# Kernel tuning notes

Measured on AMD Instinct MI355X. Metric: run time of the kernel, lower is better.

The kernel has to match this reference:

```python
import jax, jax.numpy as jnp
import numpy as np
import math

B, S, H = 8, 2048, 256

def setup_inputs() -> dict:
    key = jax.random.key(0)
    ks = jax.random.split(key, 7)
    stdv = 1.0 / math.sqrt(H)
    return {
        "k": jax.random.normal(ks[0], (B, S, H), dtype=jnp.float32),
        "q": jax.random.normal(ks[1], (B, S, H), dtype=jnp.float32),
        "v": jax.random.normal(ks[2], (B, S, H), dtype=jnp.float32),
        "mask": jax.random.bernoulli(ks[3], 0.5, (B, S, S)),  # bool, masked-out positions
        "W_query": jax.random.uniform(ks[4], (H, H), jnp.float32, -stdv, stdv),
        "W_key": jax.random.uniform(ks[5], (H, H), jnp.float32, -stdv, stdv),
        "W_val": jax.random.uniform(ks[6], (H, H), jnp.float32, -stdv, stdv),
    }

def reference(k, q, v, mask, W_query, W_key, W_val):
    Q = jnp.einsum("bsh,hd->bsd", q, W_query)
    K = jnp.einsum("bsh,hd->bsd", k, W_key)
    V = jnp.einsum("bsh,hd->bsd", v, W_val)
    norm = 1.0 / math.sqrt(Q.shape[-1])
    compat = norm * jnp.einsum("bqd,bkd->bqk", Q, K)  # [B,Sq,Sk]
    compat = jnp.where(mask, -jnp.inf, compat)
    score = jax.nn.softmax(compat, axis=-1)
    score = jnp.nan_to_num(score, nan=0.0)  # fully-masked rows -> all zeros
    return jnp.einsum("bqk,bkd->bqd", score, V)
```

## Files before the change

kernel.cpp:

```cpp
#include <hip/hip_runtime.h>


#define B_ 8
#define S_ 2048
#define H_ 256

typedef __attribute__((ext_vector_type(8))) short s16x8;
typedef __attribute__((ext_vector_type(4))) float f32x4;
typedef __attribute__((ext_vector_type(4))) unsigned short u16x4;
typedef __attribute__((ext_vector_type(8))) unsigned short u16x8;

#if __has_builtin(__builtin_amdgcn_exp2f)
#define EXP2F(x) __builtin_amdgcn_exp2f(x)
#else
#define EXP2F(x) exp2f(x)
#endif
#define L2E 1.4426950408889634f

__device__ __forceinline__ unsigned short f2bf(float f) {
  unsigned int u = __builtin_bit_cast(unsigned int, f);
  u += 0x7fffu + ((u >> 16) & 1u);
  return (unsigned short)(u >> 16);
}
__device__ __forceinline__ float bf2f(unsigned short h) {
  unsigned int u = ((unsigned int)h) << 16;
  return __builtin_bit_cast(float, u);
}
__device__ __forceinline__ f32x4 mfma_bf16(s16x8 a, s16x8 b, f32x4 c) {
  return __builtin_amdgcn_mfma_f32_16x16x32_bf16(a, b, c, 0, 0, 0);
}
__device__ __forceinline__ float sel4(const float v[4], int r) {
  float t0 = (r & 1) ? v[1] : v[0];
  float t1 = (r & 1) ? v[3] : v[2];
  return (r & 2) ? t1 : t0;
}
__device__ __forceinline__ void async16(const unsigned short* g, unsigned short* l) {
  __builtin_amdgcn_global_load_lds(
      (const __attribute__((address_space(1))) unsigned int*)g,
      (__attribute__((address_space(3))) unsigned int*)l, 16, 0, 0);
}

__global__ __launch_bounds__(256) void wt_kernel(
    const float* __restrict__ Wq, const float* __restrict__ Wk,
    const float* __restrict__ Wv, unsigned short* __restrict__ Wt) {
  __shared__ unsigned short tile[64 * 72];
  int z = blockIdx.x >> 4, x = blockIdx.x & 15;
  const float* W = (z == 0) ? Wq : (z == 1) ? Wk : Wv;
  int n0 = (x & 3) * 64, h0 = (x >> 2) * 64;
  int t = threadIdx.x;
#pragma unroll
  for (int j = 0; j < 4; ++j) {
    int c = j * 256 + t;
    int i = c >> 4, ch = c & 15;
    float4 f = *(const float4*)&W[(h0 + i) * 256 + n0 + ch * 4];
    u16x4 p;
    p[0] = f2bf(f.x); p[1] = f2bf(f.y); p[2] = f2bf(f.z); p[3] = f2bf(f.w);
    *(u16x4*)&tile[i * 72 + ch * 4] = p;
  }
  __syncthreads();
#pragma unroll
  for (int j = 0; j < 2; ++j) {
    int c = j * 256 + t;
    int nr = c >> 3, ch = c & 7;
    u16x8 o;
#pragma unroll
    for (int k = 0; k < 8; ++k) o[k] = tile[(ch * 8 + k) * 72 + nr];
    *(u16x8*)&Wt[z * 65536 + (n0 + nr) * 256 + h0 + ch * 8] = o;
  }
}

__global__ __launch_bounds__(256) void fused_kernel(
    const int* __restrict__ mask, unsigned short* __restrict__ Mb,
    const float* __restrict__ Xq, const float* __restrict__ Xk,
    const float* __restrict__ Xv, const unsigned short* __restrict__ Wt,
    unsigned short* __restrict__ Qb, unsigned short* __restrict__ Kb,
    unsigned short* __restrict__ Vt) {
  __shared__ unsigned short plds[16384];

  if (blockIdx.x >= 768) {
    unsigned int g = (blockIdx.x - 768) * 256 + threadIdx.x;
    const int4* src = (const int4*)mask + (size_t)g * 4;
    unsigned int v = 0;
#pragma unroll
    for (int j = 0; j < 4; ++j) {
      int4 x = src[j];
      v |= (x.x != 0 ? 1u : 0u) << (j * 4 + 0);
      v |= (x.y != 0 ? 1u : 0u) << (j * 4 + 1);
      v |= (x.z != 0 ? 1u : 0u) << (j * 4 + 2);
      v |= (x.w != 0 ? 1u : 0u) << (j * 4 + 3);
    }
    Mb[g] = (unsigned short)v;
    return;
  }

  int z = blockIdx.x >> 8;
  int bx = blockIdx.x & 255;
  const float* X = (z == 0) ? Xq : (z == 1) ? Xk : Xv;
  const unsigned short* Wz = Wt + z * 65536;

  int t = threadIdx.x;
  int w = t >> 6, lane = t & 63, quad = lane >> 4, l15 = lane & 15;
  int m0 = bx * 64;
  const float* xrow = X + (size_t)(m0 + w * 16 + l15) * H_;

  f32x4 zero4 = {0.f, 0.f, 0.f, 0.f};
  f32x4 acc[16];
#pragma unroll
  for (int i = 0; i < 16; ++i) acc[i] = zero4;

#pragma unroll
  for (int j = 0; j < 4; ++j) {
    int c = j * 256 + t;
    int n = c >> 2, p = c & 3;
    async16(Wz + n * 256 + ((p ^ ((n >> 1) & 3)) << 3),
            plds + j * 2048 + w * 512);
  }
  float4 a0 = *(const float4*)(xrow + quad * 8);
  float4 a1 = *(const float4*)(xrow + quad * 8 + 4);

  for (int c8 = 0; c8 < 8; ++c8) {
    int cur = c8 & 1;
    unsigned short* Wc = plds + cur * 8192;
    __syncthreads();

    if (c8 < 7) {
      unsigned short* Wn = plds + (cur ^ 1) * 8192;
#pragma unroll
      for (int j = 0; j < 4; ++j) {
        int c = j * 256 + t;
        int n = c >> 2, p = c & 3;
        async16(Wz + n * 256 + (c8 + 1) * 32 + ((p ^ ((n >> 1) & 3)) << 3),
                Wn + j * 2048 + w * 512);
      }
    }
    float4 na0, na1;
    if (c8 < 7) {
      na0 = *(const float4*)(xrow + (c8 + 1) * 32 + quad * 8);
      na1 = *(const float4*)(xrow + (c8 + 1) * 32 + quad * 8 + 4);
    }
    s16x8 af;
    af[0] = (short)f2bf(a0.x); af[1] = (short)f2bf(a0.y);
    af[2] = (short)f2bf(a0.z); af[3] = (short)f2bf(a0.w);
    af[4] = (short)f2bf(a1.x); af[5] = (short)f2bf(a1.y);
    af[6] = (short)f2bf(a1.z); af[7] = (short)f2bf(a1.w);

#pragma unroll
    for (int nf = 0; nf < 16; ++nf) {
      int n = nf * 16 + l15;
      s16x8 bf = *(const s16x8*)&Wc[n * 32 + ((quad ^ ((n >> 1) & 3)) << 3)];
      acc[nf] = mfma_bf16(af, bf, acc[nf]);
    }
    a0 = na0; a1 = na1;
  }
  __syncthreads();

  float scale = (z == 0) ? 0.0625f : 1.0f;
  int b = m0 >> 11, s0 = m0 & 2047;
#pragma unroll
  for (int h = 0; h < 2; ++h) {
    if (h) __syncthreads();
    if (z < 2) {
#pragma unroll
      for (int nf2 = 0; nf2 < 8; ++nf2) {
        int n = nf2 * 16 + l15;
#pragma unroll
        for (int r = 0; r < 4; ++r)
          plds[(w * 16 + quad * 4 + r) * 136 + n] = f2bf(acc[h * 8 + nf2][r] * scale);
      }
      __syncthreads();
      unsigned short* Y = (z == 0) ? Qb : Kb;
#pragma unroll
      for (int j = 0; j < 4; ++j) {
        int c = j * 256 + t;
        int mr = c >> 4, ch = c & 15;
        u16x8 o = *(const u16x8*)&plds[mr * 136 + ch * 8];
        *(u16x8*)&Y[(size_t)(m0 + mr) * H_ + h * 128 + ch * 8] = o;
      }
    } else {
#pragma unroll
      for (int nf2 = 0; nf2 < 8; ++nf2) {
        int dl = nf2 * 16 + l15;
#pragma unroll
        for (int r = 0; r < 4; ++r)
          plds[dl * 72 + (w * 16 + quad * 4 + r)] = f2bf(acc[h * 8 + nf2][r]);
      }
      __syncthreads();
#pragma unroll
      for (int j = 0; j < 4; ++j) {
        int c = j * 256 + t;
        int dr = c >> 3, ch = c & 7;
        u16x8 o = *(const u16x8*)&plds[dr * 72 + ch * 8];
        *(u16x8*)&Vt[((size_t)b * H_ + h * 128 + dr) * S_ + s0 + ch * 8] = o;
      }
    }
  }
}

__global__ __launch_bounds__(256, 2) void attn_kernel(
    const unsigned short* __restrict__ Qb, const unsigned short* __restrict__ Kb,
    const unsigned short* __restrict__ Vt, const unsigned int* __restrict__ Mb,
    unsigned short* __restrict__ Op, float* __restrict__ Ml,
    float* __restrict__ out) {
  __shared__ unsigned short lds[35328];
  unsigned short* Ps = lds + 32768;

  int t = threadIdx.x;
  int w = t >> 6, lane = t & 63, quad = lane >> 4, l15 = lane & 15;
  int b = blockIdx.x;
  int q0 = blockIdx.y * 64;
  int split = blockIdx.z, nsplit = gridDim.z;
  int kbeg = (64 * split) / nsplit, kend = (64 * (split + 1)) / nsplit;

  s16x8 qa[8];
  {
    const unsigned short* qp =
        Qb + ((size_t)b * S_ + q0 + w * 16 + l15) * H_ + quad * 8;
#pragma unroll
    for (int c = 0; c < 8; ++c) qa[c] = *(const s16x8*)(qp + 32 * c);
  }

  const unsigned short* Kbb = Kb + (size_t)b * S_ * H_;
  const unsigned short* Vbb = Vt + (size_t)b * H_ * S_;

  int krow = lane >> 5, kch = lane & 31;
  int vrow = lane >> 2, vch = lane & 3;

  f32x4 zero4 = {0.f, 0.f, 0.f, 0.f};
  f32x4 acc[16];
#pragma unroll
  for (int i = 0; i < 16; ++i) acc[i] = zero4;
  float l_r[4] = {0.f, 0.f, 0.f, 0.f};

  const unsigned int* mrow[4];
#pragma unroll
  for (int r = 0; r < 4; ++r)
    mrow[r] = Mb + ((size_t)b * S_ + q0 + w * 16 + quad * 4 + r) * 64;

  {
    int k0 = kbeg * 32;
    unsigned short* Kd = lds;
    unsigned short* Vd = lds + 8192;
#pragma unroll
    for (int j = 0; j < 4; ++j) {
      int key = (w * 4 + j) * 2 + krow;
      async16(Kbb + ((size_t)(k0 + key) << 8) + ((kch ^ (key & 7)) << 3),
              Kd + (w * 4 + j) * 512);
      int d = w * 64 + j * 16 + vrow;
      async16(Vbb + ((size_t)d << 11) + k0 + ((vch ^ (d & 3)) << 3),
              Vd + (w * 64 + j * 16) * 32);
    }
  }
  unsigned int mw[4];
#pragma unroll
  for (int r = 0; r < 4; ++r) mw[r] = mrow[r][kbeg];

  for (int kt = kbeg; kt < kend; ++kt) {
    int cur = (kt - kbeg) & 1;
    unsigned short* Ksc = lds + cur * 16384;
    unsigned short* Vsc = Ksc + 8192;
    __syncthreads();

    if (kt + 1 < kend) {
      int k0 = (kt + 1) * 32;
      unsigned short* Kd = lds + (cur ^ 1) * 16384;
      unsigned short* Vd = Kd + 8192;
#pragma unroll
      for (int j = 0; j < 4; ++j) {
        int key = (w * 4 + j) * 2 + krow;
        async16(Kbb + ((size_t)(k0 + key) << 8) + ((kch ^ (key & 7)) << 3),
                Kd + (w * 4 + j) * 512);
        int d = w * 64 + j * 16 + vrow;
        async16(Vbb + ((size_t)d << 11) + k0 + ((vch ^ (d & 3)) << 3),
                Vd + (w * 64 + j * 16) * 32);
      }
    }
    unsigned int mwn[4];
    {
      int ktn = (kt + 1 < kend) ? kt + 1 : kt;
#pragma unroll
      for (int r = 0; r < 4; ++r) mwn[r] = mrow[r][ktn];
    }

    f32x4 sacc[2];
#pragma unroll
    for (int nf = 0; nf < 2; ++nf) sacc[nf] = zero4;
#pragma unroll
    for (int c = 0; c < 8; ++c) {
#pragma unroll
      for (int nf = 0; nf < 2; ++nf) {
        int n = nf * 16 + l15;
        s16x8 kb = *(const s16x8*)&Ksc[n * 256 + (((quad + 4 * c) ^ (n & 7)) << 3)];
        sacc[nf] = mfma_bf16(qa[c], kb, sacc[nf]);
      }
    }

    float pvv[2][4];
#pragma unroll
    for (int r = 0; r < 4; ++r) {
      unsigned int bits = mw[r] >> l15;
#pragma unroll
      for (int nf = 0; nf < 2; ++nf) {
        float p = ((bits >> (nf * 16)) & 1u)
                      ? 0.f
                      : EXP2F(sacc[nf][r] * L2E);
        pvv[nf][r] = p;
        l_r[r] += p;
      }
    }

#pragma unroll
    for (int nf = 0; nf < 2; ++nf)
#pragma unroll
      for (int r = 0; r < 4; ++r) {
        int key = nf * 16 + l15;
        int ql = quad * 4 + r;
        Ps[w * 640 + ql * 40 + key] = f2bf(pvv[nf][r]);
      }

    {
      s16x8 bp = *(const s16x8*)&Ps[w * 640 + l15 * 40 + quad * 8];
#pragma unroll
      for (int mf = 0; mf < 16; ++mf) {
        int d = mf * 16 + l15;
        s16x8 av = *(const s16x8*)&Vsc[d * 32 + ((quad ^ (d & 3)) << 3)];
        acc[mf] = mfma_bf16(av, bp, acc[mf]);
      }
    }

#pragma unroll
    for (int r = 0; r < 4; ++r) mw[r] = mwn[r];
  }

#pragma unroll
  for (int r = 0; r < 4; ++r) {
#pragma unroll
    for (int d = 1; d < 16; d <<= 1) l_r[r] += __shfl_xor(l_r[r], d, 64);
  }

  if (gridDim.z == 1) {
    float l4[4];
    int srcl = (l15 >> 2) << 4;
#pragma unroll
    for (int r = 0; r < 4; ++r) l4[r] = __shfl(l_r[r], srcl, 64);
    float lq = sel4(l4, l15 & 3);
    float linv = (lq > 0.f) ? (1.0f / lq) : 0.f;
    float* op = out + ((size_t)b * S_ + q0 + w * 16 + l15) * H_ + quad * 4;
#pragma unroll
    for (int mf = 0; mf < 16; ++mf) {
      float4 o;
      o.x = acc[mf][0] * linv; o.y = acc[mf][1] * linv;
      o.z = acc[mf][2] * linv; o.w = acc[mf][3] * linv;
      *(float4*)(op + mf * 16) = o;
    }
  } else {
    int qg = q0 + w * 16 + l15;
    unsigned short* op =
        Op + (((size_t)split * B_ + b) * S_ + qg) * H_ + quad * 4;
#pragma unroll
    for (int mf = 0; mf < 16; ++mf) {
      u16x4 pk;
      pk[0] = f2bf(acc[mf][0]); pk[1] = f2bf(acc[mf][1]);
      pk[2] = f2bf(acc[mf][2]); pk[3] = f2bf(acc[mf][3]);
      *(u16x4*)(op + mf * 16) = pk;
    }
    if (l15 == 0) {
#pragma unroll
      for (int r = 0; r < 4; ++r) {
        int qr = q0 + w * 16 + quad * 4 + r;
        Ml[((size_t)split * B_ + b) * S_ + qr] = l_r[r];
      }
    }
  }
}

__global__ __launch_bounds__(1024) void combine_kernel(
    const unsigned short* __restrict__ Op, const float* __restrict__ Ml,
    float* __restrict__ out, int nsplit) {
  int q = blockIdx.x * 4 + (threadIdx.x >> 8);
  int b = blockIdx.y, d = threadIdx.x & 255;
  float osum = 0.f, lsum = 0.f;
  for (int i = 0; i < nsplit; ++i) {
    size_t ro = ((size_t)i * B_ + b) * S_ + q;
    lsum += Ml[ro];
    osum += bf2f(Op[ro * H_ + d]);
  }
  float linv = (lsum > 0.f) ? (1.0f / lsum) : 0.f;
  out[((size_t)b * S_ + q) * H_ + d] = osum * linv;
}

extern "C" void kernel_launch(void* const* d_in, const int* in_sizes, int n_in,
                              void* d_out, int out_size, void* d_ws, size_t ws_size,
                              hipStream_t stream) {
  const float* k_in = (const float*)d_in[0];
  const float* q_in = (const float*)d_in[1];
  const float* v_in = (const float*)d_in[2];
  const int* mask = (const int*)d_in[3];
  const float* Wq = (const float*)d_in[4];
  const float* Wk = (const float*)d_in[5];
  const float* Wv = (const float*)d_in[6];
  float* out = (float*)d_out;

  unsigned short* Qb = (unsigned short*)d_ws;
  unsigned short* Kb = Qb + (size_t)4194304;
  unsigned short* Vt = Kb + (size_t)4194304;
  unsigned short* Wt = Vt + (size_t)4194304;
  unsigned short* Mb = Wt + (size_t)196608;
  unsigned short* Op = Mb + (size_t)2097152;
  float* Ml = (float*)(Op + (size_t)8388608);
  const size_t need = 46792704;
  int nsplit = (ws_size >= need) ? 2 : 1;

  hipLaunchKernelGGL(wt_kernel, dim3(48), dim3(256), 0, stream,
                     Wq, Wk, Wv, Wt);
  hipLaunchKernelGGL(fused_kernel, dim3(8960), dim3(256), 0, stream,
                     mask, Mb, q_in, k_in, v_in, Wt, Qb, Kb, Vt);
  hipLaunchKernelGGL(attn_kernel, dim3(8, 32, nsplit), dim3(256), 0, stream,
                     Qb, Kb, Vt, (const unsigned int*)Mb, Op, Ml, out);
  if (nsplit > 1)
    hipLaunchKernelGGL(combine_kernel, dim3(512, 8), dim3(1024), 0, stream,
                       Op, Ml, out, nsplit);
}
```

Before: 311.7 us.

## Single-buffer attention LDS for higher occupancy, raise split-K to 4, ballot mask packing

The attention kernel drops K/V double buffering and uses a single LDS buffer with a sync before and after each async load. This roughly halves shared memory per block, and launch bounds now ask for 4 blocks per CU. The key dimension is split into 4 parts instead of 2, which adds more partial outputs and a larger workspace for the combine kernel. The mask packing now uses coalesced per-thread loads with a wavefront ballot instead of each thread reading 16 ints. The trade-off is that load latency is no longer overlapped inside a block, relying instead on more resident blocks and a larger grid.

```diff
diff --git a/kernel.cpp b/kernel.cpp
--- a/kernel.cpp
+++ b/kernel.cpp
@@ -77,19 +77,20 @@
     unsigned short* __restrict__ Vt) {
   __shared__ unsigned short plds[16384];
 
+  int t = threadIdx.x;
+  int w = t >> 6, lane = t & 63, quad = lane >> 4, l15 = lane & 15;
+
   if (blockIdx.x >= 768) {
-    unsigned int g = (blockIdx.x - 768) * 256 + threadIdx.x;
-    const int4* src = (const int4*)mask + (size_t)g * 4;
-    unsigned int v = 0;
-#pragma unroll
-    for (int j = 0; j < 4; ++j) {
-      int4 x = src[j];
-      v |= (x.x != 0 ? 1u : 0u) << (j * 4 + 0);
-      v |= (x.y != 0 ? 1u : 0u) << (j * 4 + 1);
-      v |= (x.z != 0 ? 1u : 0u) << (j * 4 + 2);
-      v |= (x.w != 0 ? 1u : 0u) << (j * 4 + 3);
-    }
-    Mb[g] = (unsigned short)v;
+    size_t base = (size_t)(blockIdx.x - 768) * 4096;
+#pragma unroll
+    for (int s = 0; s < 16; ++s) {
+      int x = mask[base + s * 256 + t];
+      unsigned long long bm = __ballot(x != 0);
+      if (lane < 4) {
+        Mb[(base >> 4) + s * 16 + w * 4 + lane] =
+            (unsigned short)(bm >> (16 * lane));
+      }
+    }
     return;
   }
 
@@ -98,8 +99,6 @@
   const float* X = (z == 0) ? Xq : (z == 1) ? Xk : Xv;
   const unsigned short* Wz = Wt + z * 65536;
 
-  int t = threadIdx.x;
-  int w = t >> 6, lane = t & 63, quad = lane >> 4, l15 = lane & 15;
   int m0 = bx * 64;
   const float* xrow = X + (size_t)(m0 + w * 16 + l15) * H_;
 
@@ -196,13 +195,15 @@
   }
 }
 
-__global__ __launch_bounds__(256, 2) void attn_kernel(
+__global__ __launch_bounds__(256, 4) void attn_kernel(
     const unsigned short* __restrict__ Qb, const unsigned short* __restrict__ Kb,
     const unsigned short* __restrict__ Vt, const unsigned int* __restrict__ Mb,
     unsigned short* __restrict__ Op, float* __restrict__ Ml,
     float* __restrict__ out) {
-  __shared__ unsigned short lds[35328];
-  unsigned short* Ps = lds + 32768;
+  __shared__ unsigned short lds[18944];
+  unsigned short* Ks = lds;
+  unsigned short* Vs = lds + 8192;
+  unsigned short* Ps = lds + 16384;
 
   int t = threadIdx.x;
   int w = t >> 6, lane = t & 63, quad = lane >> 4, l15 = lane & 15;
@@ -236,44 +237,24 @@
   for (int r = 0; r < 4; ++r)
     mrow[r] = Mb + ((size_t)b * S_ + q0 + w * 16 + quad * 4 + r) * 64;
 
-  {
-    int k0 = kbeg * 32;
-    unsigned short* Kd = lds;
-    unsigned short* Vd = lds + 8192;
+  unsigned int mw[4];
+#pragma unroll
+  for (int r = 0; r < 4; ++r) mw[r] = mrow[r][kbeg];
+
+  for (int kt = kbeg; kt < kend; ++kt) {
+    int k0 = kt * 32;
+    __syncthreads();
 #pragma unroll
     for (int j = 0; j < 4; ++j) {
       int key = (w * 4 + j) * 2 + krow;
       async16(Kbb + ((size_t)(k0 + key) << 8) + ((kch ^ (key & 7)) << 3),
-              Kd + (w * 4 + j) * 512);
+              Ks + (w * 4 + j) * 512);
       int d = w * 64 + j * 16 + vrow;
       async16(Vbb + ((size_t)d << 11) + k0 + ((vch ^ (d & 3)) << 3),
-              Vd + (w * 64 + j * 16) * 32);
-    }
-  }
-  unsigned int mw[4];
-#pragma unroll
-  for (int r = 0; r < 4; ++r) mw[r] = mrow[r][kbeg];
-
-  for (int kt = kbeg; kt < kend; ++kt) {
-    int cur = (kt - kbeg) & 1;
-    unsigned short* Ksc = lds + cur * 16384;
-    unsigned short* Vsc = Ksc + 8192;
+              Vs + (w * 64 + j * 16) * 32);
+    }
     __syncthreads();
 
-    if (kt + 1 < kend) {
-      int k0 = (kt + 1) * 32;
-      unsigned short* Kd = lds + (cur ^ 1) * 16384;
-      unsigned short* Vd = Kd + 8192;
-#pragma unroll
-      for (int j = 0; j < 4; ++j) {
-        int key = (w * 4 + j) * 2 + krow;
-        async16(Kbb + ((size_t)(k0 + key) << 8) + ((kch ^ (key & 7)) << 3),
-                Kd + (w * 4 + j) * 512);
-        int d = w * 64 + j * 16 + vrow;
-        async16(Vbb + ((size_t)d << 11) + k0 + ((vch ^ (d & 3)) << 3),
-                Vd + (w * 64 + j * 16) * 32);
-      }
-    }
     unsigned int mwn[4];
     {
       int ktn = (kt + 1 < kend) ? kt + 1 : kt;
@@ -289,7 +270,7 @@
 #pragma unroll
       for (int nf = 0; nf < 2; ++nf) {
         int n = nf * 16 + l15;
-        s16x8 kb = *(const s16x8*)&Ksc[n * 256 + (((quad + 4 * c) ^ (n & 7)) << 3)];
+        s16x8 kb = *(const s16x8*)&Ks[n * 256 + (((quad + 4 * c) ^ (n & 7)) << 3)];
         sacc[nf] = mfma_bf16(qa[c], kb, sacc[nf]);
       }
     }
@@ -300,9 +281,7 @@
       unsigned int bits = mw[r] >> l15;
 #pragma unroll
       for (int nf = 0; nf < 2; ++nf) {
-        float p = ((bits >> (nf * 16)) & 1u)
-                      ? 0.f
-                      : EXP2F(sacc[nf][r] * L2E);
+        float p = ((bits >> (nf * 16)) & 1u) ? 0.f : EXP2F(sacc[nf][r] * L2E);
         pvv[nf][r] = p;
         l_r[r] += p;
       }
@@ -322,7 +301,7 @@
 #pragma unroll
       for (int mf = 0; mf < 16; ++mf) {
         int d = mf * 16 + l15;
-        s16x8 av = *(const s16x8*)&Vsc[d * 32 + ((quad ^ (d & 3)) << 3)];
+        s16x8 av = *(const s16x8*)&Vs[d * 32 + ((quad ^ (d & 3)) << 3)];
         acc[mf] = mfma_bf16(av, bp, acc[mf]);
       }
     }
@@ -406,9 +385,9 @@
   unsigned short* Wt = Vt + (size_t)4194304;
   unsigned short* Mb = Wt + (size_t)196608;
   unsigned short* Op = Mb + (size_t)2097152;
-  float* Ml = (float*)(Op + (size_t)8388608);
-  const size_t need = 46792704;
-  int nsplit = (ws_size >= need) ? 2 : 1;
+  float* Ml = (float*)(Op + (size_t)16777216);
+  const size_t need = 63569920;
+  int nsplit = (ws_size >= need) ? 4 : 1;
 
   hipLaunchKernelGGL(wt_kernel, dim3(48), dim3(256), 0, stream,
                      Wq, Wk, Wv, Wt);
```

After: 473.0 us. 51.7% more time.
